# Performance work log

Measured on AMD Instinct MI355X. Metric: run time of the kernel, lower is better.

The kernel has to match this reference:

```python
import jax, jax.numpy as jnp
import numpy as np

S, D, H, DK, DV = 4096, 2048, 16, 128, 128


def setup_inputs() -> dict:
    key = jax.random.key(0)
    ks = jax.random.split(key, 9)
    s = lambda fan_in: 1.0 / np.sqrt(fan_in)
    return {
        "x": jax.random.normal(ks[0], (S, D), dtype=jnp.float32),
        "Wq": jax.random.uniform(ks[1], (H, D, DK), jnp.float32, -s(D), s(D)),
        "bq": jax.random.uniform(ks[2], (H, DK), jnp.float32, -s(D), s(D)),
        "Wk": jax.random.uniform(ks[3], (H, D, DK), jnp.float32, -s(D), s(D)),
        "bk": jax.random.uniform(ks[4], (H, DK), jnp.float32, -s(D), s(D)),
        "Wv": jax.random.uniform(ks[5], (H, D, DV), jnp.float32, -s(D), s(D)),
        "bv": jax.random.uniform(ks[6], (H, DV), jnp.float32, -s(D), s(D)),
        "Wo": jax.random.uniform(ks[7], (H * DV, D), jnp.float32, -s(H * DV), s(H * DV)),
        "bo": jax.random.uniform(ks[8], (D,), jnp.float32, -s(H * DV), s(H * DV)),
    }


def reference(x, Wq, bq, Wk, bk, Wv, bv, Wo, bo):
    # Per-head projections batched over the head axis: [H, S, dk/dv]
    q = jnp.einsum("sd,hdk->hsk", x, Wq) + bq[:, None, :]
    k = jnp.einsum("sd,hdk->hsk", x, Wk) + bk[:, None, :]
    v = jnp.einsum("sd,hdv->hsv", x, Wv) + bv[:, None, :]
    # Scaled dot-product attention per head (mask=None path)
    scores = jnp.einsum("hqk,hsk->hqs", q, k) / jnp.sqrt(jnp.asarray(DK, x.dtype))
    attn = jax.nn.softmax(scores, axis=-1)          # [H, S, S]
    out = jnp.einsum("hqs,hsv->hqv", attn, v)       # [H, S, dv]
    # torch.cat(..., dim=1): interleave heads on feature dim -> [S, H*dv]
    cat = jnp.transpose(out, (1, 0, 2)).reshape(S, H * DV)
    return cat @ Wo + bo
```

## Files before the change

### kernel.cpp

```cpp
#include <hip/hip_runtime.h>
#include <hip/hip_bf16.h>

typedef __attribute__((ext_vector_type(8))) short bhalf8;
typedef __attribute__((ext_vector_type(4))) short bhalf4;
typedef __attribute__((ext_vector_type(4))) float f32x4;
typedef __attribute__((ext_vector_type(16))) float f32x16;
typedef __attribute__((ext_vector_type(4))) unsigned int u32x4;

#define S_SEQ 4096
#define DMODEL 2048
#define NHEAD 16
#define DHEAD 128

__device__ __forceinline__ short f2bf(float f) {
  union { float f; unsigned int u; } v; v.f = f;
  unsigned int r = v.u + 0x7fffu + ((v.u >> 16) & 1u);
  return (short)(r >> 16);
}

__device__ __forceinline__ unsigned pk2(float a, float b) {
  union { __hip_bfloat16 h; unsigned short u; } x, y;
  x.h = __float2bfloat16(a); y.h = __float2bfloat16(b);
  return (unsigned)x.u | ((unsigned)y.u << 16);
}

__global__ __launch_bounds__(256) void k_convert(const float* __restrict__ in,
                                                 short* __restrict__ out, int n4) {
  int i = blockIdx.x * 256 + threadIdx.x;
  if (i >= n4) return;
  f32x4 v = ((const f32x4*)in)[i];
  bhalf4 o;
  o[0] = f2bf(v[0]); o[1] = f2bf(v[1]); o[2] = f2bf(v[2]); o[3] = f2bf(v[3]);
  ((bhalf4*)out)[i] = o;
}

__global__ __launch_bounds__(256) void k_transpose(const float* __restrict__ in,
                                                   short* __restrict__ out, int R, int C) {
  long bs = (long)R * C;
  const float* inp = in + (long)blockIdx.y * bs;
  short* outp = out + (long)blockIdx.y * bs;
  int ct = C >> 6;
  int r0 = (blockIdx.x / ct) << 6;
  int c0 = (blockIdx.x % ct) << 6;
  __shared__ float T[64][65];
  int tid = threadIdx.x;
#pragma unroll
  for (int i = 0; i < 4; i++) {
    int chunk = tid + i * 256;
    int r = chunk >> 4, c = (chunk & 15) << 2;
    f32x4 v = *(const f32x4*)(inp + (long)(r0 + r) * C + c0 + c);
    T[r][c] = v[0]; T[r][c + 1] = v[1]; T[r][c + 2] = v[2]; T[r][c + 3] = v[3];
  }
  __syncthreads();
#pragma unroll
  for (int i = 0; i < 4; i++) {
    int chunk = tid + i * 256;
    int oc = chunk >> 4, o4 = (chunk & 15) << 2;
    bhalf4 o;
    o[0] = f2bf(T[o4][oc]);     o[1] = f2bf(T[o4 + 1][oc]);
    o[2] = f2bf(T[o4 + 2][oc]); o[3] = f2bf(T[o4 + 3][oc]);
    *(bhalf4*)(outp + (long)(c0 + oc) * R + r0 + o4) = o;
  }
}

template <int MODE>
__global__ __launch_bounds__(256) void k_gemm(const short* __restrict__ A, int lda, long a_bs,
                                              const short* __restrict__ Bt, int ldb, long b_bs,
                                              void* __restrict__ Cp, int ldc, long c_bs,
                                              const float* __restrict__ bias, int bias_bs,
                                              float alpha,
                                              int Mtiles, int Ntiles, int K) {
  const int b = blockIdx.y;
  A += (long)b * a_bs;
  Bt += (long)b * b_bs;
  bias += (long)b * bias_bs;
  int bx = blockIdx.x;
  if (gridDim.y == 1) bx = (bx & 7) * (gridDim.x >> 3) + (bx >> 3);
  const int mt = bx / Ntiles, nt = bx % Ntiles;
  const int row0 = mt << 7, col0 = nt << 7;
  const int tid = threadIdx.x;
  const int wave = tid >> 6, lane = tid & 63;
  const int wr = wave >> 1, wc = wave & 1;
  const int lr = lane & 15, lg = lane >> 4;

  __shared__ short As[128][72];
  __shared__ short Bs[128][72];

  f32x4 acc[4][4];
#pragma unroll
  for (int mi = 0; mi < 4; mi++)
#pragma unroll
    for (int ni = 0; ni < 4; ni++) acc[mi][ni] = (f32x4){0.f, 0.f, 0.f, 0.f};

  for (int k0 = 0; k0 < K; k0 += 64) {
    __syncthreads();
#pragma unroll
    for (int i = 0; i < 4; i++) {
      int chunk = tid + i * 256;
      int r = chunk >> 3, c = (chunk & 7) << 3;
      *(bhalf8*)&As[r][c] = *(const bhalf8*)(A + (long)(row0 + r) * lda + k0 + c);
      *(bhalf8*)&Bs[r][c] = *(const bhalf8*)(Bt + (long)(col0 + r) * ldb + k0 + c);
    }
    __syncthreads();
#pragma unroll
    for (int kk = 0; kk < 2; kk++) {
      bhalf8 af[4], bf[4];
#pragma unroll
      for (int mi = 0; mi < 4; mi++)
        af[mi] = *(const bhalf8*)&As[wr * 64 + mi * 16 + lr][kk * 32 + lg * 8];
#pragma unroll
      for (int ni = 0; ni < 4; ni++)
        bf[ni] = *(const bhalf8*)&Bs[wc * 64 + ni * 16 + lr][kk * 32 + lg * 8];
#pragma unroll
      for (int mi = 0; mi < 4; mi++)
#pragma unroll
        for (int ni = 0; ni < 4; ni++)
          acc[mi][ni] = __builtin_amdgcn_mfma_f32_16x16x32_bf16(af[mi], bf[ni], acc[mi][ni], 0, 0, 0);
    }
  }

#pragma unroll
  for (int mi = 0; mi < 4; mi++) {
#pragma unroll
    for (int ni = 0; ni < 4; ni++) {
#pragma unroll
      for (int r = 0; r < 4; r++) {
        int row = row0 + wr * 64 + mi * 16 + lg * 4 + r;
        int col = col0 + wc * 64 + ni * 16 + lr;
        float v = acc[mi][ni][r];
        if (MODE == 0) {
          v = (v + bias[col]) * alpha;
          ((short*)Cp)[(long)b * c_bs + (long)row * ldc + col] = f2bf(v);
        } else if (MODE == 1) {
          v = (v + bias[row]) * alpha;
          ((short*)Cp)[(long)b * c_bs + (long)row * ldc + col] = f2bf(v);
        } else {
          v += bias[col];
          ((float*)Cp)[(long)b * c_bs + (long)row * ldc + col] = v;
        }
      }
    }
  }
}

__global__ __launch_bounds__(512, 2) void k_attn(const short* __restrict__ q,
                                                 const short* __restrict__ k,
                                                 const short* __restrict__ vT,
                                                 short* __restrict__ cat) {
  __shared__ __align__(16) char smem[98304];
  const int wg = blockIdx.x;
  const int wgid = (wg & 7) * 32 + (wg >> 3);
  const int h = wgid >> 4;
  const int q0 = (wgid & 15) << 8;
  const int tid = threadIdx.x;
  const int wave = tid >> 6;
  const int l31 = tid & 31;
  const int hi = (tid >> 5) & 1;
  const int swl = (tid & 15) << 4;

  const long qk_base = (long)h * S_SEQ * DHEAD;
  const long vt_base = (long)h * DHEAD * S_SEQ;

  {
    u32x4 qst[8];
#pragma unroll
    for (int r = 0; r < 8; r++) {
      int o = r * 8192 + tid * 16;
      int row = o >> 8, col = o & 255;
      qst[r] = *(const u32x4*)(q + qk_base + (long)(q0 + row) * DHEAD + (col >> 1));
    }
#pragma unroll
    for (int r = 0; r < 8; r++) {
      int o = r * 8192 + tid * 16;
      int row = o >> 8, col = o & 255;
      *(u32x4*)(smem + row * 256 + (col ^ ((row & 15) << 4))) = qst[r];
    }
  }
  __syncthreads();
  bhalf8 qf[8];
#pragma unroll
  for (int kc = 0; kc < 8; kc++) {
    int row = wave * 32 + l31;
    qf[kc] = *(const bhalf8*)(smem + row * 256 + ((kc * 32 + hi * 16) ^ swl));
  }
  __syncthreads();

  f32x16 accO[4];
#pragma unroll
  for (int d = 0; d < 4; d++)
#pragma unroll
    for (int r = 0; r < 16; r++) accO[d][r] = 0.f;
  float m_run = -1e30f, l_part = 0.f;

  u32x4 st[4];
  auto load_tile = [&](int kv0) {
#pragma unroll
    for (int r2 = 0; r2 < 2; r2++) {
      int o = r2 * 8192 + tid * 16;
      int row = o >> 8, col = o & 255;
      st[r2] = *(const u32x4*)(k + qk_base + (long)(kv0 + row) * DHEAD + (col >> 1));
    }
#pragma unroll
    for (int r2 = 0; r2 < 2; r2++) {
      int o = r2 * 8192 + tid * 16;
      int dv = o >> 7, col = o & 127;
      st[2 + r2] = *(const u32x4*)(vT + vt_base + (long)dv * S_SEQ + kv0 + (col >> 1));
    }
  };
  auto write_tile = [&](char* buf) {
#pragma unroll
    for (int r2 = 0; r2 < 2; r2++) {
      int o = r2 * 8192 + tid * 16;
      int row = o >> 8, col = o & 255;
      *(u32x4*)(buf + row * 256 + (col ^ ((row & 15) << 4))) = st[r2];
    }
#pragma unroll
    for (int r2 = 0; r2 < 2; r2++) {
      int o = r2 * 8192 + tid * 16;
      int dv = o >> 7, col = o & 127;
      *(u32x4*)(buf + 16384 + (dv & 63) * 256 +
                ((((dv >> 6) << 7) + col) ^ ((dv & 15) << 4))) = st[2 + r2];
    }
  };

  auto qkt = [&](f32x16 (&acc)[2], const char* buf) {
#pragma unroll
    for (int kvb = 0; kvb < 2; kvb++)
#pragma unroll
      for (int r = 0; r < 16; r++) acc[kvb][r] = 0.f;
    __builtin_amdgcn_s_setprio(1);
#pragma unroll
    for (int kvb = 0; kvb < 2; kvb++) {
      int row = kvb * 32 + l31;
#pragma unroll
      for (int kc = 0; kc < 8; kc++) {
        bhalf8 kf = *(const bhalf8*)(buf + row * 256 + ((kc * 32 + hi * 16) ^ swl));
        acc[kvb] = __builtin_amdgcn_mfma_f32_32x32x16_bf16(kf, qf[kc], acc[kvb], 0, 0, 0);
      }
    }
    __builtin_amdgcn_s_setprio(0);
  };

  auto sm_pv = [&](f32x16 (&accS)[2], const char* buf) {
    float mx[8];
#pragma unroll
    for (int g = 0; g < 8; g++) {
      const int kvb = g >> 2, b4 = (g & 3) * 4;
      mx[g] = fmaxf(fmaxf(accS[kvb][b4], accS[kvb][b4 + 1]),
                    fmaxf(accS[kvb][b4 + 2], accS[kvb][b4 + 3]));
    }
    float mc = fmaxf(fmaxf(fmaxf(mx[0], mx[1]), fmaxf(mx[2], mx[3])),
                     fmaxf(fmaxf(mx[4], mx[5]), fmaxf(mx[6], mx[7])));
    mc = fmaxf(mc, __shfl_xor(mc, 32));

    if (!__all(mc <= m_run + 8.f)) {
      float mn = fmaxf(m_run, mc);
      float corr = __builtin_amdgcn_exp2f(m_run - mn);
      m_run = mn;
      l_part *= corr;
#pragma unroll
      for (int d = 0; d < 4; d++)
#pragma unroll
        for (int r = 0; r < 16; r++) accO[d][r] *= corr;
    }

    unsigned pk[2][4][2];
#pragma unroll
    for (int kvb = 0; kvb < 2; kvb++)
#pragma unroll
      for (int g = 0; g < 4; g++) {
        float p0 = __builtin_amdgcn_exp2f(accS[kvb][4 * g + 0] - m_run);
        float p1 = __builtin_amdgcn_exp2f(accS[kvb][4 * g + 1] - m_run);
        float p2 = __builtin_amdgcn_exp2f(accS[kvb][4 * g + 2] - m_run);
        float p3 = __builtin_amdgcn_exp2f(accS[kvb][4 * g + 3] - m_run);
        l_part += (p0 + p1) + (p2 + p3);
        pk[kvb][g][0] = pk2(p0, p1);
        pk[kvb][g][1] = pk2(p2, p3);
      }

    bhalf8 pa[4];
#pragma unroll
    for (int kvb = 0; kvb < 2; kvb++)
#pragma unroll
      for (int c1 = 0; c1 < 2; c1++) {
        unsigned a0 = pk[kvb][2 * c1][0],     a1 = pk[kvb][2 * c1][1];
        unsigned b0 = pk[kvb][2 * c1 + 1][0], b1 = pk[kvb][2 * c1 + 1][1];
        unsigned s0a = (unsigned)__shfl_xor((int)a0, 32);
        unsigned s1a = (unsigned)__shfl_xor((int)a1, 32);
        unsigned s0b = (unsigned)__shfl_xor((int)b0, 32);
        unsigned s1b = (unsigned)__shfl_xor((int)b1, 32);
        union { unsigned u[4]; bhalf8 v; } cvt;
        cvt.u[0] = hi ? s0b : a0;
        cvt.u[1] = hi ? s1b : a1;
        cvt.u[2] = hi ? b0 : s0a;
        cvt.u[3] = hi ? b1 : s1a;
        pa[kvb * 2 + c1] = cvt.v;
      }

    __builtin_amdgcn_s_setprio(1);
#pragma unroll
    for (int d = 0; d < 4; d++) {
      int vrow = ((d & 1) << 5) + l31;
      int vhalf = (d >> 1) << 7;
#pragma unroll
      for (int c = 0; c < 4; c++) {
        bhalf8 vf = *(const bhalf8*)(buf + 16384 + vrow * 256 +
                                     ((vhalf + c * 32 + hi * 16) ^ swl));
        accO[d] = __builtin_amdgcn_mfma_f32_32x32x16_bf16(vf, pa[c], accO[d], 0, 0, 0);
      }
    }
    __builtin_amdgcn_s_setprio(0);
  };

  f32x16 accA[2], accB[2];

  load_tile(0);
  write_tile(smem);
  load_tile(64);
  __syncthreads();
  qkt(accA, smem);
  write_tile(smem + 32768);
  load_tile(128);

  const int NT = S_SEQ / 64;
  int bc = 0, bn = 32768, bw = 65536;
  auto phase = [&](f32x16 (&cur)[2], f32x16 (&nxt)[2], int t) {
    __syncthreads();
    if (t + 1 < NT) qkt(nxt, smem + bn);
    sm_pv(cur, smem + bc);
    if (t + 2 < NT) write_tile(smem + bw);
    if (t + 3 < NT) load_tile((t + 3) * 64);
    int tmp = bc; bc = bn; bn = bw; bw = tmp;
  };

  for (int tp = 0; tp < NT / 2; tp++) {
    phase(accA, accB, 2 * tp);
    phase(accB, accA, 2 * tp + 1);
  }

  float l_tot = l_part + __shfl_xor(l_part, 32);
  float inv = 1.f / l_tot;
  long rowbase = (long)(q0 + wave * 32 + l31) * DMODEL + h * DHEAD;
#pragma unroll
  for (int d = 0; d < 4; d++)
#pragma unroll
    for (int rg = 0; rg < 4; rg++) {
      bhalf4 ov;
#pragma unroll
      for (int i = 0; i < 4; i++) ov[i] = f2bf(accO[d][rg * 4 + i] * inv);
      *(bhalf4*)(cat + rowbase + d * 32 + rg * 8 + hi * 4) = ov;
    }
}

extern "C" void kernel_launch(void* const* d_in, const int* in_sizes, int n_in,
                              void* d_out, int out_size, void* d_ws, size_t ws_size,
                              hipStream_t stream) {
  const float* x  = (const float*)d_in[0];
  const float* Wq = (const float*)d_in[1];
  const float* bq = (const float*)d_in[2];
  const float* Wk = (const float*)d_in[3];
  const float* bk = (const float*)d_in[4];
  const float* Wv = (const float*)d_in[5];
  const float* bv = (const float*)d_in[6];
  const float* Wo = (const float*)d_in[7];
  const float* bo = (const float*)d_in[8];
  float* out = (float*)d_out;

  short* x_bf   = (short*)d_ws;
  short* Wqt    = x_bf  + (long)S_SEQ * DMODEL;
  short* Wkt    = Wqt   + (long)NHEAD * DHEAD * DMODEL;
  short* Wvt    = Wkt   + (long)NHEAD * DHEAD * DMODEL;
  short* Wot    = Wvt   + (long)NHEAD * DHEAD * DMODEL;
  short* q_bf   = Wot   + (long)DMODEL * DMODEL;
  short* k_bf   = q_bf  + (long)NHEAD * S_SEQ * DHEAD;
  short* vT_bf  = k_bf  + (long)NHEAD * S_SEQ * DHEAD;
  short* cat_bf = vT_bf + (long)NHEAD * DHEAD * S_SEQ;

  dim3 blk(256);

  k_convert<<<dim3((S_SEQ * DMODEL / 4 + 255) / 256), blk, 0, stream>>>(x, x_bf, S_SEQ * DMODEL / 4);

  k_transpose<<<dim3((DMODEL / 64) * (DHEAD / 64), NHEAD), blk, 0, stream>>>(Wq, Wqt, DMODEL, DHEAD);
  k_transpose<<<dim3((DMODEL / 64) * (DHEAD / 64), NHEAD), blk, 0, stream>>>(Wk, Wkt, DMODEL, DHEAD);
  k_transpose<<<dim3((DMODEL / 64) * (DHEAD / 64), NHEAD), blk, 0, stream>>>(Wv, Wvt, DMODEL, DHEAD);
  k_transpose<<<dim3((DMODEL / 64) * (DMODEL / 64), 1), blk, 0, stream>>>(Wo, Wot, DMODEL, DMODEL);

  const float alpha_q = 0.08838834764831845f * 1.4426950408889634f;

  k_gemm<0><<<dim3(32, NHEAD), blk, 0, stream>>>(x_bf, DMODEL, 0L,
                                                 Wqt, DMODEL, (long)DHEAD * DMODEL,
                                                 q_bf, DHEAD, (long)S_SEQ * DHEAD,
                                                 bq, DHEAD, alpha_q, 32, 1, DMODEL);
  k_gemm<0><<<dim3(32, NHEAD), blk, 0, stream>>>(x_bf, DMODEL, 0L,
                                                 Wkt, DMODEL, (long)DHEAD * DMODEL,
                                                 k_bf, DHEAD, (long)S_SEQ * DHEAD,
                                                 bk, DHEAD, 1.0f, 32, 1, DMODEL);
  k_gemm<1><<<dim3(32, NHEAD), blk, 0, stream>>>(Wvt, DMODEL, (long)DHEAD * DMODEL,
                                                 x_bf, DMODEL, 0L,
                                                 vT_bf, S_SEQ, (long)DHEAD * S_SEQ,
                                                 bv, DHEAD, 1.0f, 1, 32, DMODEL);

  k_attn<<<dim3(256), dim3(512), 0, stream>>>(q_bf, k_bf, vT_bf, cat_bf);

  k_gemm<2><<<dim3(32 * 16, 1), blk, 0, stream>>>(cat_bf, DMODEL, 0L,
                                                  Wot, DMODEL, 0L,
                                                  out, DMODEL, 0L,
                                                  bo, 0, 1.0f, 32, 16, DMODEL);
}
```

Before: 356.8 us.

## Permute V tile columns at load to drop P-fragment cross-lane shuffles

```diff
diff --git a/kernel.cpp b/kernel.cpp
--- a/kernel.cpp
+++ b/kernel.cpp
@@ -6,6 +6,7 @@
 typedef __attribute__((ext_vector_type(4))) float f32x4;
 typedef __attribute__((ext_vector_type(16))) float f32x16;
 typedef __attribute__((ext_vector_type(4))) unsigned int u32x4;
+typedef __attribute__((ext_vector_type(2))) unsigned int u32x2;
 
 #define S_SEQ 4096
 #define DMODEL 2048
@@ -192,19 +193,28 @@
     for (int r = 0; r < 16; r++) accO[d][r] = 0.f;
   float m_run = -1e30f, l_part = 0.f;
 
-  u32x4 st[4];
+  u32x4 stk[2];
+  u32x2 stv[4];
   auto load_tile = [&](int kv0) {
 #pragma unroll
     for (int r2 = 0; r2 < 2; r2++) {
       int o = r2 * 8192 + tid * 16;
       int row = o >> 8, col = o & 255;
-      st[r2] = *(const u32x4*)(k + qk_base + (long)(kv0 + row) * DHEAD + (col >> 1));
+      stk[r2] = *(const u32x4*)(k + qk_base + (long)(kv0 + row) * DHEAD + (col >> 1));
     }
 #pragma unroll
     for (int r2 = 0; r2 < 2; r2++) {
       int o = r2 * 8192 + tid * 16;
       int dv = o >> 7, col = o & 127;
-      st[2 + r2] = *(const u32x4*)(vT + vt_base + (long)dv * S_SEQ + kv0 + (col >> 1));
+      int slot0 = col >> 1;
+#pragma unroll
+      for (int h2 = 0; h2 < 2; h2++) {
+        int slot = slot0 + h2 * 4;
+        int g = (slot >> 2) & 3;
+        int gs = ((g & 1) << 1) | (g >> 1);
+        int aslot = (slot & ~15) | (gs << 2);
+        stv[r2 * 2 + h2] = *(const u32x2*)(vT + vt_base + (long)dv * S_SEQ + kv0 + aslot);
+      }
     }
   };
   auto write_tile = [&](char* buf) {
@@ -212,14 +222,17 @@
     for (int r2 = 0; r2 < 2; r2++) {
       int o = r2 * 8192 + tid * 16;
       int row = o >> 8, col = o & 255;
-      *(u32x4*)(buf + row * 256 + (col ^ ((row & 15) << 4))) = st[r2];
+      *(u32x4*)(buf + row * 256 + (col ^ ((row & 15) << 4))) = stk[r2];
     }
 #pragma unroll
     for (int r2 = 0; r2 < 2; r2++) {
       int o = r2 * 8192 + tid * 16;
       int dv = o >> 7, col = o & 127;
+      u32x4 w;
+      w[0] = stv[r2 * 2][0];     w[1] = stv[r2 * 2][1];
+      w[2] = stv[r2 * 2 + 1][0]; w[3] = stv[r2 * 2 + 1][1];
       *(u32x4*)(buf + 16384 + (dv & 63) * 256 +
-                ((((dv >> 6) << 7) + col) ^ ((dv & 15) << 4))) = st[2 + r2];
+                ((((dv >> 6) << 7) + col) ^ ((dv & 15) << 4))) = w;
     }
   };
 
@@ -283,17 +296,11 @@
     for (int kvb = 0; kvb < 2; kvb++)
 #pragma unroll
       for (int c1 = 0; c1 < 2; c1++) {
-        unsigned a0 = pk[kvb][2 * c1][0],     a1 = pk[kvb][2 * c1][1];
-        unsigned b0 = pk[kvb][2 * c1 + 1][0], b1 = pk[kvb][2 * c1 + 1][1];
-        unsigned s0a = (unsigned)__shfl_xor((int)a0, 32);
-        unsigned s1a = (unsigned)__shfl_xor((int)a1, 32);
-        unsigned s0b = (unsigned)__shfl_xor((int)b0, 32);
-        unsigned s1b = (unsigned)__shfl_xor((int)b1, 32);
         union { unsigned u[4]; bhalf8 v; } cvt;
-        cvt.u[0] = hi ? s0b : a0;
-        cvt.u[1] = hi ? s1b : a1;
-        cvt.u[2] = hi ? b0 : s0a;
-        cvt.u[3] = hi ? b1 : s1a;
+        cvt.u[0] = pk[kvb][2 * c1][0];
+        cvt.u[1] = pk[kvb][2 * c1][1];
+        cvt.u[2] = pk[kvb][2 * c1 + 1][0];
+        cvt.u[3] = pk[kvb][2 * c1 + 1][1];
         pa[kvb * 2 + c1] = cvt.v;
       }
 
```

Measured after the change: 347.8 us. -2.5%, faster.
